# Kernel tuning notes

Hardware: AMD Instinct MI355X
Metric: run time of the kernel (lower is better)

## Reference

```python
import jax, jax.numpy as jnp
import numpy as np

EPS = 1e-8

def _rasterize_mesh(face_verts, H, W):
    # face_verts: [F,3,3] = (ndc_x, ndc_y, view_z) per triangle vertex
    x0, y0, z0 = face_verts[:, 0, 0], face_verts[:, 0, 1], face_verts[:, 0, 2]
    x1, y1, z1 = face_verts[:, 1, 0], face_verts[:, 1, 1], face_verts[:, 1, 2]
    x2, y2, z2 = face_verts[:, 2, 0], face_verts[:, 2, 1], face_verts[:, 2, 2]
    area = (x1 - x0) * (y2 - y0) - (y1 - y0) * (x2 - x0)
    # cull_backfaces=True (area<=0) + degenerate + behind-camera cull
    face_ok = (area > EPS) & (z0 > 0) & (z1 > 0) & (z2 > 0)
    inv_area = jnp.where(face_ok, 1.0 / jnp.where(face_ok, area, 1.0), 0.0)
    zs = jnp.stack([z0, z1, z2], -1)  # [F,3]
    # pytorch3d NDC: +x left, +y up, pixel centers
    xs = 1.0 - (2.0 * jnp.arange(W, dtype=jnp.float32) + 1.0) / W
    ys = 1.0 - (2.0 * jnp.arange(H, dtype=jnp.float32) + 1.0) / H

    def row_fn(py):
        px = xs[:, None]  # [W,1] broadcast vs faces [F]
        w0 = ((x1 - px) * (y2 - py) - (y1 - py) * (x2 - px)) * inv_area
        w1 = ((x2 - px) * (y0 - py) - (y2 - py) * (x0 - px)) * inv_area
        w2 = ((x0 - px) * (y1 - py) - (y0 - py) * (x1 - px)) * inv_area
        inside = (w0 >= 0) & (w1 >= 0) & (w2 >= 0) & face_ok
        # perspective_correct=True: l_i = w_i * prod(other z), renormalize
        l = jnp.stack([w0 * z1 * z2, z0 * w1 * z2, z0 * z1 * w2], -1)  # [W,F,3]
        s = l.sum(-1, keepdims=True)
        b = l / jnp.where(s == 0, 1.0, s)
        # clip_barycentric_coords=True
        b = jnp.clip(b, 0.0, None)
        b = b / jnp.clip(b.sum(-1, keepdims=True), EPS, None)
        zpix = (b * zs[None]).sum(-1)  # [W,F] interpolated view-space depth
        zm = jnp.where(inside, zpix, jnp.inf)
        fidx = jnp.argmin(zm, axis=1)  # z-buffer winner per pixel
        zmin = jnp.take_along_axis(zm, fidx[:, None], 1)[:, 0]
        hit = jnp.isfinite(zmin)
        bary = jnp.take_along_axis(b, fidx[:, None, None], 1)[:, 0]  # [W,3]
        return (jnp.where(hit, fidx, -1),
                jnp.where(hit, zmin, -1.0),
                jnp.where(hit[:, None], bary, -1.0))

    return jax.lax.map(row_fn, ys)  # ([H,W],[H,W],[H,W,3])


def _forward(positions, features, faces, K, RT, H, W):
    B, V, _ = positions.shape
    Fn = faces.shape[1]
    # --- create_camera_objects: open3d/opencv KRT -> pytorch3d camera ---
    R = RT[:, :, :3]
    t = RT[:, :, 3]
    scale = min(H, W) / 2.0
    focal = jnp.stack([K[:, 0, 0], K[:, 1, 1]], -1) / scale  # [B,2] NDC focal
    p0 = -(jnp.stack([K[:, 0, 2], K[:, 1, 2]], -1)
           - jnp.array([W / 2.0, H / 2.0], jnp.float32)) / scale  # [B,2]
    sign = jnp.array([-1.0, -1.0, 1.0], jnp.float32)
    R_p = jnp.swapaxes(R, 1, 2) * sign[None, None, :]  # R^T with cols 0,1 negated
    T_p = t * sign[None, :]
    # --- _get_mesh_ndc: world -> view -> NDC (pytorch3d row-vector convention) ---
    v_view = jnp.einsum('bvi,bij->bvj', positions, R_p) + T_p[:, None, :]
    z = v_view[..., 2:3]
    xy_ndc = focal[:, None, :] * v_view[..., :2] / z + p0[:, None, :]
    verts_ndc = jnp.concatenate([xy_ndc, z], -1)  # z overwritten with view-space depth
    face_verts = jax.vmap(lambda v, f: v[f])(verts_ndc, faces)  # [B,F,3,3]
    # --- rasterize (blur_sigma=0 -> faces_per_pixel=1) ---
    p2f, zbuf, bary = jax.vmap(lambda fv: _rasterize_mesh(fv, H, W))(face_verts)
    hit = p2f >= 0
    pix_to_face = jnp.where(hit, p2f + (jnp.arange(B) * Fn)[:, None, None], -1)
    # --- interpolate_face_attributes on packed faces/verts ---
    faces_packed = (faces + (jnp.arange(B) * V)[:, None, None]).reshape(B * Fn, 3)
    feats_packed = features.reshape(B * V, -1)
    fv_idx = faces_packed[jnp.clip(pix_to_face, 0)]  # [B,H,W,3]
    attrs = feats_packed[fv_idx]                      # [B,H,W,3,C]
    pix_feats = (bary[..., None] * attrs).sum(-2)
    pix_feats = jnp.where(hit[..., None], pix_feats, 0.0)
    dists = jnp.where(hit, 0.0, -1.0)
    # add faces_per_pixel (K=1) axis, matching pytorch3d Fragments layout
    return (pix_feats[:, :, :, None, :], pix_to_face[:, :, :, None],
            zbuf[:, :, :, None], bary[:, :, :, None, :], dists[:, :, :, None])


def setup_inputs() -> dict:
    key = jax.random.key(0)
    k1, k2, k3 = jax.random.split(key, 3)
    B, V, Fn, C, H, W = 1, 8192, 16384, 64, 192, 192
    positions = jax.random.uniform(k1, (B, V, 3), jnp.float32) * 2.0 - 1.0
    features = jax.random.normal(k2, (B, V, C), jnp.float32)
    faces = jax.random.randint(k3, (B, Fn, 3), 0, V)
    K = jnp.broadcast_to(jnp.array([[180.0, 0.0, 96.0], [0.0, 180.0, 96.0],
                                    [0.0, 0.0, 1.0]], jnp.float32), (B, 3, 3))
    RT = jnp.broadcast_to(jnp.concatenate(
        [jnp.eye(3, dtype=jnp.float32),
         jnp.array([[0.0], [0.0], [3.5]], jnp.float32)], axis=1), (B, 3, 4))
    return {"positions": positions, "features": features, "faces": faces,
            "K": K, "RT": RT, "H": H, "W": W, "blur_sigma": 0}


def reference(positions, features, faces, K, RT, H, W, blur_sigma):
    # blur_sigma == 0 path of VertexShader.forward (faces_per_pixel=1)
    return _forward(positions, features, faces, K, RT, H, W)
```

## Files before the change

### kernel.cpp

```cpp
#include <hip/hip_runtime.h>
#include <stdint.h>

#define H_ 192
#define W_ 192
#define C_ 64
#define EPS_F 1e-8f
#define TILE 16
#define NTX (W_/TILE)
#define NTY (H_/TILE)
#define CHUNK 256
#define NSLICE 8
#define NBUCKET 256
#define MAXCHUNK 64

typedef unsigned long long ull;

#define OFF_FEATS 0
#define OFF_P2F   (H_*W_*C_)
#define OFF_ZBUF  (OFF_P2F + H_*W_)
#define OFF_BARY  (OFF_ZBUF + H_*W_)
#define OFF_DIST  (OFF_BARY + H_*W_*3)

__device__ __forceinline__ float xm(float a, float b){ return __fmul_rn(a,b); }
__device__ __forceinline__ float xa(float a, float b){ return __fadd_rn(a,b); }
__device__ __forceinline__ float xsb(float a, float b){ return __fsub_rn(a,b); }
__device__ __forceinline__ float xd(float a, float b){ return __fdiv_rn(a,b); }

__device__ __forceinline__ float pixcoord(int i, float dim){
    float t = xa(xm(2.0f, (float)i), 1.0f);
    return xsb(1.0f, xd(t, dim));
}

__device__ __forceinline__ unsigned fenc(float f){
    unsigned b = __float_as_uint(f);
    return (b & 0x80000000u) ? ~b : (b | 0x80000000u);
}
__device__ __forceinline__ float fdec(unsigned e){
    unsigned b = (e & 0x80000000u) ? (e & 0x7FFFFFFFu) : ~e;
    return __uint_as_float(b);
}

__device__ __forceinline__ int zbucket(float zmn){
    int b = (int)((zmn - 2.0f) * 64.0f);
    return b < 0 ? 0 : (b > 254 ? 254 : b);
}
__device__ __forceinline__ float zlo_bucket(int b){
    if (b >= 255) return INFINITY;
    if (b == 0)   return 0.0f;
    return 2.0f + (float)b * 0.015625f;
}

__device__ __forceinline__ float3 tv(const float* __restrict__ pos,
        const float* __restrict__ K, const float* __restrict__ RT, int i){
    float p0 = pos[3*i+0], p1 = pos[3*i+1], p2 = pos[3*i+2];
    const float sgn[3] = {-1.f, -1.f, 1.f};
    float vv[3];
    #pragma unroll
    for (int j=0;j<3;j++){
        float rp0 = xm(RT[j*4+0], sgn[j]);
        float rp1 = xm(RT[j*4+1], sgn[j]);
        float rp2 = xm(RT[j*4+2], sgn[j]);
        float s = xa(xa(xm(p0,rp0), xm(p1,rp1)), xm(p2,rp2));
        vv[j] = xa(s, xm(RT[j*4+3], sgn[j]));
    }
    float z = vv[2];
    float fx = xd(K[0], 96.0f);
    float fy = xd(K[4], 96.0f);
    float p0x = -xd(xsb(K[2], 96.0f), 96.0f);
    float p0y = -xd(xsb(K[5], 96.0f), 96.0f);
    float xn = xa(xd(xm(fx, vv[0]), z), p0x);
    float yn = xa(xd(xm(fy, vv[1]), z), p0y);
    return make_float3(xn, yn, z);
}

__global__ __launch_bounds__(64) void k_pre(const float* __restrict__ pos,
        const float* __restrict__ K, const float* __restrict__ RT,
        const int* __restrict__ faces, float* __restrict__ rec0,
        unsigned* __restrict__ hist, unsigned* __restrict__ gbbmin,
        unsigned* __restrict__ gbbmax, int Fn){
    __shared__ unsigned lh[NBUCKET];
    int t = threadIdx.x, B = blockIdx.x;
    #pragma unroll
    for (int i=t; i<NBUCKET; i+=64) lh[i] = 0u;
    __syncthreads();
    int f = B*64 + t;
    float bxmn=INFINITY, bxmx=-INFINITY, bymn=INFINITY, bymx=-INFINITY;
    if (f < Fn){
        int i0 = faces[3*f+0], i1 = faces[3*f+1], i2 = faces[3*f+2];
        float3 v0 = tv(pos,K,RT,i0), v1 = tv(pos,K,RT,i1), v2 = tv(pos,K,RT,i2);
        float area = xsb(xm(xsb(v1.x,v0.x), xsb(v2.y,v0.y)), xm(xsb(v1.y,v0.y), xsb(v2.x,v0.x)));
        bool ok = (area > EPS_F) && (v0.z > 0.f) && (v1.z > 0.f) && (v2.z > 0.f);
        float ia = ok ? xd(1.0f, area) : 0.0f;
        float zmn = INFINITY;
        int b = 255;
        if (ok){
            zmn = fminf(v0.z, fminf(v1.z, v2.z));
            b = zbucket(zmn);
            bxmn = fminf(v0.x, fminf(v1.x, v2.x)) - 1e-4f;
            bxmx = fmaxf(v0.x, fmaxf(v1.x, v2.x)) + 1e-4f;
            bymn = fminf(v0.y, fminf(v1.y, v2.y)) - 1e-4f;
            bymx = fmaxf(v0.y, fmaxf(v1.y, v2.y)) + 1e-4f;
        }
        atomicAdd(&lh[b], 1u);
        float4* q = (float4*)(rec0 + (size_t)f*12);
        q[0] = make_float4(v0.x, v0.y, v1.x, v1.y);
        q[1] = make_float4(v2.x, v2.y, v0.z, v1.z);
        q[2] = make_float4(v2.z, ia, __int_as_float(f), zmn);
    }
    #pragma unroll
    for (int s2=1; s2<64; s2<<=1){
        bxmn = fminf(bxmn, __shfl_xor(bxmn, s2, 64));
        bxmx = fmaxf(bxmx, __shfl_xor(bxmx, s2, 64));
        bymn = fminf(bymn, __shfl_xor(bymn, s2, 64));
        bymx = fmaxf(bymx, __shfl_xor(bymx, s2, 64));
    }
    if (t == 0){
        atomicMin(&gbbmin[0], fenc(bxmn));
        atomicMax(&gbbmax[0], fenc(bxmx));
        atomicMin(&gbbmin[1], fenc(bymn));
        atomicMax(&gbbmax[1], fenc(bymx));
    }
    __syncthreads();
    #pragma unroll
    for (int i=t; i<NBUCKET; i+=64){
        unsigned cc = lh[i];
        if (cc) atomicAdd(&hist[i], cc);
    }
}

__global__ __launch_bounds__(256) void k_scatter(const float* __restrict__ rec0,
        const unsigned* __restrict__ hist, unsigned* __restrict__ histcur,
        float* __restrict__ rec, float* __restrict__ suffz, int Fn){
    __shared__ unsigned gst[NBUCKET], ssc[NBUCKET], lcnt[NBUCKET], lbase[NBUCKET];
    int t = threadIdx.x, B = blockIdx.x;
    unsigned hv = hist[t];
    ssc[t] = hv;
    lcnt[t] = 0u;
    __syncthreads();
    for (int d=1; d<NBUCKET; d<<=1){
        unsigned u = (t >= d) ? ssc[t-d] : 0u;
        __syncthreads();
        ssc[t] += u;
        __syncthreads();
    }
    gst[t] = ssc[t] - hv;
    __syncthreads();
    if (B == 0 && t < MAXCHUNK){
        unsigned pos = (unsigned)t * CHUNK;
        int bb = 0;
        #pragma unroll
        for (int s = 128; s > 0; s >>= 1){
            int nb = bb + s;
            if (nb <= NBUCKET && ssc[nb-1] <= pos) bb = nb;
        }
        suffz[t] = zlo_bucket(bb);
    }
    int f = B*256 + t;
    bool valid = (f < Fn);
    float4 q0, q1, q2;
    int b = 255; unsigned rank = 0; bool ok = false; float zmn = INFINITY;
    if (valid){
        const float4* q = (const float4*)(rec0 + (size_t)f*12);
        q0 = q[0]; q1 = q[1]; q2 = q[2];
        ok = (q2.y > 0.f);
        zmn = q2.w;
        b = ok ? zbucket(zmn) : 255;
        rank = atomicAdd(&lcnt[b], 1u);
    }
    __syncthreads();
    unsigned add = lcnt[t];
    if (add) lbase[t] = atomicAdd(&histcur[t], add);
    __syncthreads();
    if (valid){
        float x0=q0.x, y0=q0.y, x1=q0.z, y1=q0.w;
        float x2=q1.x, y2=q1.y, z0=q1.z, z1=q1.w;
        float z2=q2.x, ia=q2.y;
        float xmn, xmx, ymn, ymx, Ap=0.f, Bp=0.f, Cp=0.f;
        if (ok){
            xmn = fminf(x0, fminf(x1, x2)) - 1e-4f;
            xmx = fmaxf(x0, fmaxf(x1, x2)) + 1e-4f;
            ymn = fminf(y0, fminf(y1, y2)) - 1e-4f;
            ymx = fmaxf(y0, fmaxf(y1, y2)) + 1e-4f;
            float iz0 = 1.f/z0, iz1 = 1.f/z1, iz2 = 1.f/z2;
            Ap = ia * ((y1-y2)*iz0 + (y2-y0)*iz1 + (y0-y1)*iz2);
            Bp = ia * ((x2-x1)*iz0 + (x0-x2)*iz1 + (x1-x0)*iz2);
            Cp = ia * ((x1*y2-x2*y1)*iz0 + (x2*y0-x0*y2)*iz1 + (x0*y1-x1*y0)*iz2);
        } else {
            xmn = INFINITY; xmx = -INFINITY; ymn = INFINITY; ymx = -INFINITY;
        }
        unsigned p = gst[b] + lbase[b] + rank;
        float4* qo = (float4*)(rec + (size_t)p*20);
        qo[0] = q0; qo[1] = q1; qo[2] = q2;
        qo[3] = make_float4(Ap, Bp, Cp, 0.f);
        qo[4] = make_float4(xmn, xmx, ymn, ymx);
    }
}

__global__ __launch_bounds__(256) void k_raster(const float* __restrict__ rec,
        const float* __restrict__ suffz, const unsigned* __restrict__ gbbmin,
        const unsigned* __restrict__ gbbmax, ull* __restrict__ keys, int Fn){
    __shared__ float lds[CHUNK*12];
    __shared__ float zl[CHUNK];
    __shared__ int   slist[CHUNK];
    __shared__ int   wcnt[4];
    __shared__ float suff[MAXCHUNK];
    int tid = threadIdx.x;
    int nchunk = (Fn + CHUNK - 1) / CHUNK;
    if (tid < MAXCHUNK) suff[tid] = suffz[tid];
    int ix = blockIdx.x*TILE + (tid & 15);
    int iy = blockIdx.y*TILE + (tid >> 4);
    int pix = iy*W_ + ix;
    float px = pixcoord(ix, (float)W_);
    float py = pixcoord(iy, (float)H_);
    float tx_hi = pixcoord(blockIdx.x*TILE,          (float)W_);
    float tx_lo = pixcoord(blockIdx.x*TILE + TILE-1, (float)W_);
    float ty_hi = pixcoord(blockIdx.y*TILE,          (float)H_);
    float ty_lo = pixcoord(blockIdx.y*TILE + TILE-1, (float)H_);
    float gx0 = fdec(gbbmin[0]), gx1 = fdec(gbbmax[0]);
    float gy0 = fdec(gbbmin[1]), gy1 = fdec(gbbmax[1]);
    bool alive = (px >= gx0) && (px <= gx1) && (py >= gy0) && (py <= gy1);
    int lane = tid & 63, wv = tid >> 6;

    float zcut = INFINITY;
    ull localkey = 0xFFFFFFFFFFFFFFFFULL;
    ull published = 0xFFFFFFFFFFFFFFFFULL;
    __syncthreads();

    for (int c = (int)blockIdx.z; c < nchunk; c += NSLICE){
        ull g = __hip_atomic_load(&keys[pix], __ATOMIC_RELAXED, __HIP_MEMORY_SCOPE_AGENT);
        float zg = __uint_as_float((unsigned)(g >> 32));
        zcut = fminf(zcut, zg);
        float sc = (c < MAXCHUNK) ? suff[c] : 0.0f;
        int done = (!alive || !(xm(sc, 0.999f) < zcut)) ? 1 : 0;
        if (__syncthreads_and(done)) break;

        int fi = c*CHUNK + tid;
        float4 q0 = make_float4(0,0,0,0), q1 = q0, q2 = q0;
        bool keep = false;
        float zb = 0.f;
        if (fi < Fn){
            const float4* gq = (const float4*)(rec + (size_t)fi*20);
            q0 = gq[0]; q1 = gq[1]; q2 = gq[2];
            float4 q3 = gq[3], q4 = gq[4];
            keep = (q4.x <= tx_hi) && (q4.y >= tx_lo) && (q4.z <= ty_hi) && (q4.w >= ty_lo);
            if (keep){
                float ax = (q3.x > 0.f) ? tx_hi : tx_lo;
                float by = (q3.y > 0.f) ? ty_hi : ty_lo;
                float Nmax = q3.z + q3.x*ax + q3.y*by;
                float M = fabsf(q3.x*ax) + fabsf(q3.y*by) + fabsf(q3.z);
                float Nub = Nmax + 1e-5f*M + 1e-30f;
                if (Nub <= 0.f) keep = false;
                else zb = fmaxf(1.f/Nub, q2.w);
            }
        }
        float4* l = (float4*)(lds + tid*12);
        l[0] = q0; l[1] = q1; l[2] = q2;
        ull m = __ballot(keep);
        if (lane == 0) wcnt[wv] = __popcll(m);
        __syncthreads();
        int basecnt = 0;
        #pragma unroll
        for (int w2 = 0; w2 < 4; ++w2) if (w2 < wv) basecnt += wcnt[w2];
        if (keep){
            int p = basecnt + __popcll(m & ((1ULL << lane) - 1ULL));
            slist[p] = tid;
            zl[p] = zb;
        }
        int nsurv = wcnt[0] + wcnt[1] + wcnt[2] + wcnt[3];
        __syncthreads();

        for (int k = 0; k < nsurv; k++){
            float zbl = zl[k];
            if (!(xm(zbl, 0.999f) < zcut)) continue;
            int j = slist[k];
            const float* r = lds + j*12;
            float x0=r[0], y0=r[1], x1=r[2], y1=r[3], x2=r[4], y2=r[5];
            float dx0=xsb(x0,px), dx1=xsb(x1,px), dx2=xsb(x2,px);
            float dy0=xsb(y0,py), dy1=xsb(y1,py), dy2=xsb(y2,py);
            float e0 = xsb(xm(dx1,dy2), xm(dy1,dx2));
            float e1 = xsb(xm(dx2,dy0), xm(dy2,dx0));
            float e2 = xsb(xm(dx0,dy1), xm(dy0,dx1));
            if (e0 >= 0.f && e1 >= 0.f && e2 >= 0.f){
                float z0=r[6], z1=r[7], z2=r[8], ia=r[9];
                float w0 = xm(e0, ia), w1 = xm(e1, ia), w2 = xm(e2, ia);
                float l0 = xm(xm(w0,z1),z2);
                float l1 = xm(xm(z0,w1),z2);
                float l2 = xm(xm(z0,z1),w2);
                float s  = xa(xa(l0,l1),l2);
                float za = (l0*z0 + l1*z1 + l2*z2) / s;
                if (za*0.99999f >= zcut) continue;
                float dn = (s == 0.f) ? 1.0f : s;
                float b0 = fmaxf(xd(l0,dn), 0.f);
                float b1 = fmaxf(xd(l1,dn), 0.f);
                float b2 = fmaxf(xd(l2,dn), 0.f);
                float bs = fmaxf(xa(xa(b0,b1),b2), EPS_F);
                b0 = xd(b0,bs); b1 = xd(b1,bs); b2 = xd(b2,bs);
                float zp = xa(xa(xm(b0,z0),xm(b1,z1)),xm(b2,z2));
                ull ck = (((ull)__float_as_uint(zp)) << 32) | (unsigned)__float_as_int(r[10]);
                if (ck < localkey) localkey = ck;
                zcut = fminf(zcut, zp);
            }
        }
        if (localkey < published){
            atomicMin(&keys[pix], localkey);
            published = localkey;
        }
    }
    if (localkey < published) atomicMin(&keys[pix], localkey);
}

__global__ __launch_bounds__(256) void k_post(const ull* __restrict__ keys,
        const float* __restrict__ rec0, const float* __restrict__ feats,
        const int* __restrict__ faces, float* __restrict__ out){
    int grp = threadIdx.x >> 6;
    int c = threadIdx.x & 63;
    int pix = blockIdx.x*4 + grp;
    float* p2f  = out + OFF_P2F;
    float* zbuf = out + OFF_ZBUF;
    float* bary = out + OFF_BARY;
    float* dist = out + OFF_DIST;
    ull key = keys[pix];
    if (key == 0xFFFFFFFFFFFFFFFFULL){
        out[OFF_FEATS + pix*C_ + c] = 0.0f;
        if (c == 0){
            p2f[pix] = -1.0f; zbuf[pix] = -1.0f; dist[pix] = -1.0f;
        }
        if (c < 3) bary[3*pix+c] = -1.0f;
        return;
    }
    int f = (int)(key & 0xFFFFFFFFu);
    float z = __uint_as_float((unsigned)(key >> 32));
    int ix = pix % W_, iy = pix / W_;
    float px = pixcoord(ix, (float)W_);
    float py = pixcoord(iy, (float)H_);
    const float4* q = (const float4*)(rec0 + (size_t)f*12);
    float4 q0 = q[0], q1 = q[1], q2 = q[2];
    float x0=q0.x, y0=q0.y, x1=q0.z, y1=q0.w;
    float x2=q1.x, y2=q1.y, z0=q1.z, z1=q1.w;
    float z2=q2.x, ia=q2.y;
    float w0 = xm(xsb(xm(xsb(x1,px),xsb(y2,py)), xm(xsb(y1,py),xsb(x2,px))), ia);
    float w1 = xm(xsb(xm(xsb(x2,px),xsb(y0,py)), xm(xsb(y2,py),xsb(x0,px))), ia);
    float w2 = xm(xsb(xm(xsb(x0,px),xsb(y1,py)), xm(xsb(y0,py),xsb(x1,px))), ia);
    float l0 = xm(xm(w0,z1),z2);
    float l1 = xm(xm(z0,w1),z2);
    float l2 = xm(xm(z0,z1),w2);
    float s  = xa(xa(l0,l1),l2);
    float dn = (s == 0.f) ? 1.0f : s;
    float b0 = fmaxf(xd(l0,dn), 0.f);
    float b1 = fmaxf(xd(l1,dn), 0.f);
    float b2 = fmaxf(xd(l2,dn), 0.f);
    float bs = fmaxf(xa(xa(b0,b1),b2), EPS_F);
    b0 = xd(b0,bs); b1 = xd(b1,bs); b2 = xd(b2,bs);
    int i0 = faces[3*f+0], i1 = faces[3*f+1], i2 = faces[3*f+2];
    float res = xa(xa(xm(b0, feats[i0*C_ + c]), xm(b1, feats[i1*C_ + c])),
                   xm(b2, feats[i2*C_ + c]));
    out[OFF_FEATS + pix*C_ + c] = res;
    if (c == 0){
        p2f[pix] = (float)f; zbuf[pix] = z; dist[pix] = 0.0f;
    }
    if (c < 3){
        float bb = (c == 0) ? b0 : ((c == 1) ? b1 : b2);
        bary[3*pix+c] = bb;
    }
}

extern "C" void kernel_launch(void* const* d_in, const int* in_sizes, int n_in,
                              void* d_out, int out_size, void* d_ws, size_t ws_size,
                              hipStream_t stream) {
    const float* positions = (const float*)d_in[0];
    const float* features  = (const float*)d_in[1];
    const int*   faces     = (const int*)  d_in[2];
    const float* K         = (const float*)d_in[3];
    const float* RT        = (const float*)d_in[4];
    int Fn = in_sizes[2] / 3;

    ull*      keys     = (ull*)d_ws;
    unsigned* gbbmin   = (unsigned*)(keys + H_*W_);
    unsigned* hist     = gbbmin + 4;
    unsigned* histcur  = hist + NBUCKET;
    unsigned* gbbmax   = histcur + NBUCKET;
    float*    suffz    = (float*)(gbbmax + 4);
    float*    rec      = suffz + MAXCHUNK;
    float*    rec0     = rec + (size_t)Fn*20;

    size_t regA = (size_t)H_*W_*sizeof(ull) + 16;
    size_t regB = (NBUCKET*2 + 4)*4;
    hipMemsetAsync(keys, 0xFF, regA, stream);
    hipMemsetAsync(hist, 0x00, regB, stream);

    int nfb = (Fn + 255) / 256;
    k_pre<<<(Fn+63)/64, 64, 0, stream>>>(positions, K, RT, faces, rec0, hist, gbbmin, gbbmax, Fn);
    k_scatter<<<nfb, 256, 0, stream>>>(rec0, hist, histcur, rec, suffz, Fn);
    dim3 rg(NTX, NTY, NSLICE);
    k_raster<<<rg, dim3(256,1,1), 0, stream>>>(rec, suffz, gbbmin, gbbmax, keys, Fn);
    k_post<<<(H_*W_)/4, 256, 0, stream>>>(keys, rec0, features, faces, (float*)d_out);
}
```

Before: 141.9 us.

## Fuse post-shading into raster via last-slice tile counter, init keys in pre-pass

```diff
diff --git a/kernel.cpp b/kernel.cpp
--- a/kernel.cpp
+++ b/kernel.cpp
@@ -8,6 +8,7 @@
 #define TILE 16
 #define NTX (W_/TILE)
 #define NTY (H_/TILE)
+#define NTILES (NTX*NTY)
 #define CHUNK 256
 #define NSLICE 8
 #define NBUCKET 256
@@ -76,10 +77,12 @@
 __global__ __launch_bounds__(64) void k_pre(const float* __restrict__ pos,
         const float* __restrict__ K, const float* __restrict__ RT,
         const int* __restrict__ faces, float* __restrict__ rec0,
-        unsigned* __restrict__ hist, unsigned* __restrict__ gbbmin,
-        unsigned* __restrict__ gbbmax, int Fn){
+        unsigned* __restrict__ hist, unsigned* __restrict__ gbb,
+        ull* __restrict__ keys, int Fn){
     __shared__ unsigned lh[NBUCKET];
     int t = threadIdx.x, B = blockIdx.x;
+    int gthreads = gridDim.x*64;
+    for (int i = B*64 + t; i < H_*W_; i += gthreads) keys[i] = 0xFFFFFFFFFFFFFFFFULL;
     #pragma unroll
     for (int i=t; i<NBUCKET; i+=64) lh[i] = 0u;
     __syncthreads();
@@ -114,11 +117,11 @@
         bymn = fminf(bymn, __shfl_xor(bymn, s2, 64));
         bymx = fmaxf(bymx, __shfl_xor(bymx, s2, 64));
     }
-    if (t == 0){
-        atomicMin(&gbbmin[0], fenc(bxmn));
-        atomicMax(&gbbmax[0], fenc(bxmx));
-        atomicMin(&gbbmin[1], fenc(bymn));
-        atomicMax(&gbbmax[1], fenc(bymx));
+    if (t == 0 && bxmx > -INFINITY){
+        atomicMax(&gbb[0], fenc(-bxmn));
+        atomicMax(&gbb[1], fenc( bxmx));
+        atomicMax(&gbb[2], fenc(-bymn));
+        atomicMax(&gbb[3], fenc( bymx));
     }
     __syncthreads();
     #pragma unroll
@@ -197,13 +200,16 @@
 }
 
 __global__ __launch_bounds__(256) void k_raster(const float* __restrict__ rec,
-        const float* __restrict__ suffz, const unsigned* __restrict__ gbbmin,
-        const unsigned* __restrict__ gbbmax, ull* __restrict__ keys, int Fn){
+        const float* __restrict__ suffz, const unsigned* __restrict__ gbb,
+        ull* __restrict__ keys, unsigned* __restrict__ tilecnt,
+        const float* __restrict__ rec0, const float* __restrict__ feats,
+        const int* __restrict__ faces, float* __restrict__ out, int Fn){
     __shared__ float lds[CHUNK*12];
     __shared__ float zl[CHUNK];
     __shared__ int   slist[CHUNK];
     __shared__ int   wcnt[4];
     __shared__ float suff[MAXCHUNK];
+    __shared__ int   lastflag;
     int tid = threadIdx.x;
     int nchunk = (Fn + CHUNK - 1) / CHUNK;
     if (tid < MAXCHUNK) suff[tid] = suffz[tid];
@@ -216,8 +222,8 @@
     float tx_lo = pixcoord(blockIdx.x*TILE + TILE-1, (float)W_);
     float ty_hi = pixcoord(blockIdx.y*TILE,          (float)H_);
     float ty_lo = pixcoord(blockIdx.y*TILE + TILE-1, (float)H_);
-    float gx0 = fdec(gbbmin[0]), gx1 = fdec(gbbmax[0]);
-    float gy0 = fdec(gbbmin[1]), gy1 = fdec(gbbmax[1]);
+    float gx0 = -fdec(gbb[0]), gx1 = fdec(gbb[1]);
+    float gy0 = -fdec(gbb[2]), gy1 = fdec(gbb[3]);
     bool alive = (px >= gx0) && (px <= gx1) && (py >= gy0) && (py <= gy1);
     int lane = tid & 63, wv = tid >> 6;
 
@@ -307,60 +313,64 @@
         }
     }
     if (localkey < published) atomicMin(&keys[pix], localkey);
-}
-
-__global__ __launch_bounds__(256) void k_post(const ull* __restrict__ keys,
-        const float* __restrict__ rec0, const float* __restrict__ feats,
-        const int* __restrict__ faces, float* __restrict__ out){
-    int grp = threadIdx.x >> 6;
-    int c = threadIdx.x & 63;
-    int pix = blockIdx.x*4 + grp;
+
+    __threadfence();
+    if (tid == 0){
+        unsigned o = atomicAdd(&tilecnt[blockIdx.y*NTX + blockIdx.x], 1u);
+        lastflag = (o == NSLICE-1) ? 1 : 0;
+    }
+    __syncthreads();
+    if (!lastflag) return;
+    __threadfence();
+
+    int grp = tid >> 6, c = tid & 63;
     float* p2f  = out + OFF_P2F;
     float* zbuf = out + OFF_ZBUF;
     float* bary = out + OFF_BARY;
     float* dist = out + OFF_DIST;
-    ull key = keys[pix];
-    if (key == 0xFFFFFFFFFFFFFFFFULL){
-        out[OFF_FEATS + pix*C_ + c] = 0.0f;
-        if (c == 0){
-            p2f[pix] = -1.0f; zbuf[pix] = -1.0f; dist[pix] = -1.0f;
-        }
-        if (c < 3) bary[3*pix+c] = -1.0f;
-        return;
-    }
-    int f = (int)(key & 0xFFFFFFFFu);
-    float z = __uint_as_float((unsigned)(key >> 32));
-    int ix = pix % W_, iy = pix / W_;
-    float px = pixcoord(ix, (float)W_);
-    float py = pixcoord(iy, (float)H_);
-    const float4* q = (const float4*)(rec0 + (size_t)f*12);
-    float4 q0 = q[0], q1 = q[1], q2 = q[2];
-    float x0=q0.x, y0=q0.y, x1=q0.z, y1=q0.w;
-    float x2=q1.x, y2=q1.y, z0=q1.z, z1=q1.w;
-    float z2=q2.x, ia=q2.y;
-    float w0 = xm(xsb(xm(xsb(x1,px),xsb(y2,py)), xm(xsb(y1,py),xsb(x2,px))), ia);
-    float w1 = xm(xsb(xm(xsb(x2,px),xsb(y0,py)), xm(xsb(y2,py),xsb(x0,px))), ia);
-    float w2 = xm(xsb(xm(xsb(x0,px),xsb(y1,py)), xm(xsb(y0,py),xsb(x1,px))), ia);
-    float l0 = xm(xm(w0,z1),z2);
-    float l1 = xm(xm(z0,w1),z2);
-    float l2 = xm(xm(z0,z1),w2);
-    float s  = xa(xa(l0,l1),l2);
-    float dn = (s == 0.f) ? 1.0f : s;
-    float b0 = fmaxf(xd(l0,dn), 0.f);
-    float b1 = fmaxf(xd(l1,dn), 0.f);
-    float b2 = fmaxf(xd(l2,dn), 0.f);
-    float bs = fmaxf(xa(xa(b0,b1),b2), EPS_F);
-    b0 = xd(b0,bs); b1 = xd(b1,bs); b2 = xd(b2,bs);
-    int i0 = faces[3*f+0], i1 = faces[3*f+1], i2 = faces[3*f+2];
-    float res = xa(xa(xm(b0, feats[i0*C_ + c]), xm(b1, feats[i1*C_ + c])),
-                   xm(b2, feats[i2*C_ + c]));
-    out[OFF_FEATS + pix*C_ + c] = res;
-    if (c == 0){
-        p2f[pix] = (float)f; zbuf[pix] = z; dist[pix] = 0.0f;
-    }
-    if (c < 3){
-        float bb = (c == 0) ? b0 : ((c == 1) ? b1 : b2);
-        bary[3*pix+c] = bb;
+    for (int pp = 0; pp < 64; ++pp){
+        int pixloc = pp*4 + grp;
+        int ix2 = blockIdx.x*TILE + (pixloc & 15);
+        int iy2 = blockIdx.y*TILE + (pixloc >> 4);
+        int pix2 = iy2*W_ + ix2;
+        ull key = __hip_atomic_load(&keys[pix2], __ATOMIC_RELAXED, __HIP_MEMORY_SCOPE_AGENT);
+        if (key == 0xFFFFFFFFFFFFFFFFULL){
+            out[OFF_FEATS + pix2*C_ + c] = 0.0f;
+            if (c == 0){ p2f[pix2] = -1.0f; zbuf[pix2] = -1.0f; dist[pix2] = -1.0f; }
+            if (c < 3) bary[3*pix2+c] = -1.0f;
+            continue;
+        }
+        int f = (int)(key & 0xFFFFFFFFu);
+        float z = __uint_as_float((unsigned)(key >> 32));
+        float px2 = pixcoord(ix2, (float)W_);
+        float py2 = pixcoord(iy2, (float)H_);
+        const float4* q = (const float4*)(rec0 + (size_t)f*12);
+        float4 q0 = q[0], q1 = q[1], q2 = q[2];
+        float x0=q0.x, y0=q0.y, x1=q0.z, y1=q0.w;
+        float x2=q1.x, y2=q1.y, z0=q1.z, z1=q1.w;
+        float z2=q2.x, ia=q2.y;
+        float w0 = xm(xsb(xm(xsb(x1,px2),xsb(y2,py2)), xm(xsb(y1,py2),xsb(x2,px2))), ia);
+        float w1 = xm(xsb(xm(xsb(x2,px2),xsb(y0,py2)), xm(xsb(y2,py2),xsb(x0,px2))), ia);
+        float w2 = xm(xsb(xm(xsb(x0,px2),xsb(y1,py2)), xm(xsb(y0,py2),xsb(x1,px2))), ia);
+        float l0 = xm(xm(w0,z1),z2);
+        float l1 = xm(xm(z0,w1),z2);
+        float l2 = xm(xm(z0,z1),w2);
+        float s  = xa(xa(l0,l1),l2);
+        float dn = (s == 0.f) ? 1.0f : s;
+        float b0 = fmaxf(xd(l0,dn), 0.f);
+        float b1 = fmaxf(xd(l1,dn), 0.f);
+        float b2 = fmaxf(xd(l2,dn), 0.f);
+        float bs = fmaxf(xa(xa(b0,b1),b2), EPS_F);
+        b0 = xd(b0,bs); b1 = xd(b1,bs); b2 = xd(b2,bs);
+        int i0 = faces[3*f+0], i1 = faces[3*f+1], i2 = faces[3*f+2];
+        float res = xa(xa(xm(b0, feats[i0*C_ + c]), xm(b1, feats[i1*C_ + c])),
+                       xm(b2, feats[i2*C_ + c]));
+        out[OFF_FEATS + pix2*C_ + c] = res;
+        if (c == 0){ p2f[pix2] = (float)f; zbuf[pix2] = z; dist[pix2] = 0.0f; }
+        if (c < 3){
+            float bb = (c == 0) ? b0 : ((c == 1) ? b1 : b2);
+            bary[3*pix2+c] = bb;
+        }
     }
 }
 
@@ -375,23 +385,21 @@
     int Fn = in_sizes[2] / 3;
 
     ull*      keys     = (ull*)d_ws;
-    unsigned* gbbmin   = (unsigned*)(keys + H_*W_);
-    unsigned* hist     = gbbmin + 4;
+    unsigned* hist     = (unsigned*)(keys + H_*W_);
     unsigned* histcur  = hist + NBUCKET;
-    unsigned* gbbmax   = histcur + NBUCKET;
-    float*    suffz    = (float*)(gbbmax + 4);
+    unsigned* gbb      = histcur + NBUCKET;
+    unsigned* tilecnt  = gbb + 4;
+    float*    suffz    = (float*)(tilecnt + NTILES);
     float*    rec      = suffz + MAXCHUNK;
     float*    rec0     = rec + (size_t)Fn*20;
 
-    size_t regA = (size_t)H_*W_*sizeof(ull) + 16;
-    size_t regB = (NBUCKET*2 + 4)*4;
-    hipMemsetAsync(keys, 0xFF, regA, stream);
+    size_t regB = (NBUCKET*2 + 4 + NTILES)*4;
     hipMemsetAsync(hist, 0x00, regB, stream);
 
     int nfb = (Fn + 255) / 256;
-    k_pre<<<(Fn+63)/64, 64, 0, stream>>>(positions, K, RT, faces, rec0, hist, gbbmin, gbbmax, Fn);
+    k_pre<<<(Fn+63)/64, 64, 0, stream>>>(positions, K, RT, faces, rec0, hist, gbb, keys, Fn);
     k_scatter<<<nfb, 256, 0, stream>>>(rec0, hist, histcur, rec, suffz, Fn);
     dim3 rg(NTX, NTY, NSLICE);
-    k_raster<<<rg, dim3(256,1,1), 0, stream>>>(rec, suffz, gbbmin, gbbmax, keys, Fn);
-    k_post<<<(H_*W_)/4, 256, 0, stream>>>(keys, rec0, features, faces, (float*)d_out);
-}
+    k_raster<<<rg, dim3(256,1,1), 0, stream>>>(rec, suffz, gbb, keys, tilecnt,
+                                               rec0, features, faces, (float*)d_out, Fn);
+}
```

Result: slower. 255.5 us (+80.1%).

## Fold key init into preprocess, merge bbox atomics, add wave-level early break in raster

Applied to the files above, without the earlier changes.

```diff
diff --git a/kernel.cpp b/kernel.cpp
--- a/kernel.cpp
+++ b/kernel.cpp
@@ -76,10 +76,12 @@
 __global__ __launch_bounds__(64) void k_pre(const float* __restrict__ pos,
         const float* __restrict__ K, const float* __restrict__ RT,
         const int* __restrict__ faces, float* __restrict__ rec0,
-        unsigned* __restrict__ hist, unsigned* __restrict__ gbbmin,
-        unsigned* __restrict__ gbbmax, int Fn){
+        unsigned* __restrict__ hist, unsigned* __restrict__ gbb,
+        ull* __restrict__ keys, int Fn){
     __shared__ unsigned lh[NBUCKET];
     int t = threadIdx.x, B = blockIdx.x;
+    int gthreads = gridDim.x*64;
+    for (int i = B*64 + t; i < H_*W_; i += gthreads) keys[i] = 0xFFFFFFFFFFFFFFFFULL;
     #pragma unroll
     for (int i=t; i<NBUCKET; i+=64) lh[i] = 0u;
     __syncthreads();
@@ -114,11 +116,11 @@
         bymn = fminf(bymn, __shfl_xor(bymn, s2, 64));
         bymx = fmaxf(bymx, __shfl_xor(bymx, s2, 64));
     }
-    if (t == 0){
-        atomicMin(&gbbmin[0], fenc(bxmn));
-        atomicMax(&gbbmax[0], fenc(bxmx));
-        atomicMin(&gbbmin[1], fenc(bymn));
-        atomicMax(&gbbmax[1], fenc(bymx));
+    if (t == 0 && bxmx > -INFINITY){
+        atomicMax(&gbb[0], fenc(-bxmn));
+        atomicMax(&gbb[1], fenc( bxmx));
+        atomicMax(&gbb[2], fenc(-bymn));
+        atomicMax(&gbb[3], fenc( bymx));
     }
     __syncthreads();
     #pragma unroll
@@ -197,10 +199,11 @@
 }
 
 __global__ __launch_bounds__(256) void k_raster(const float* __restrict__ rec,
-        const float* __restrict__ suffz, const unsigned* __restrict__ gbbmin,
-        const unsigned* __restrict__ gbbmax, ull* __restrict__ keys, int Fn){
+        const float* __restrict__ suffz, const unsigned* __restrict__ gbb,
+        ull* __restrict__ keys, int Fn){
     __shared__ float lds[CHUNK*12];
     __shared__ float zl[CHUNK];
+    __shared__ float zfs[CHUNK];
     __shared__ int   slist[CHUNK];
     __shared__ int   wcnt[4];
     __shared__ float suff[MAXCHUNK];
@@ -216,8 +219,8 @@
     float tx_lo = pixcoord(blockIdx.x*TILE + TILE-1, (float)W_);
     float ty_hi = pixcoord(blockIdx.y*TILE,          (float)H_);
     float ty_lo = pixcoord(blockIdx.y*TILE + TILE-1, (float)H_);
-    float gx0 = fdec(gbbmin[0]), gx1 = fdec(gbbmax[0]);
-    float gy0 = fdec(gbbmin[1]), gy1 = fdec(gbbmax[1]);
+    float gx0 = -fdec(gbb[0]), gx1 = fdec(gbb[1]);
+    float gy0 = -fdec(gbb[2]), gy1 = fdec(gbb[3]);
     bool alive = (px >= gx0) && (px <= gx1) && (py >= gy0) && (py <= gy1);
     int lane = tid & 63, wv = tid >> 6;
 
@@ -237,7 +240,7 @@
         int fi = c*CHUNK + tid;
         float4 q0 = make_float4(0,0,0,0), q1 = q0, q2 = q0;
         bool keep = false;
-        float zb = 0.f;
+        float zb = 0.f, zf = 0.f;
         if (fi < Fn){
             const float4* gq = (const float4*)(rec + (size_t)fi*20);
             q0 = gq[0]; q1 = gq[1]; q2 = gq[2];
@@ -250,7 +253,10 @@
                 float M = fabsf(q3.x*ax) + fabsf(q3.y*by) + fabsf(q3.z);
                 float Nub = Nmax + 1e-5f*M + 1e-30f;
                 if (Nub <= 0.f) keep = false;
-                else zb = fmaxf(1.f/Nub, q2.w);
+                else {
+                    zf = zlo_bucket(zbucket(q2.w));
+                    zb = fmaxf(fmaxf(1.f/Nub, q2.w), zf);
+                }
             }
         }
         float4* l = (float4*)(lds + tid*12);
@@ -265,11 +271,14 @@
             int p = basecnt + __popcll(m & ((1ULL << lane) - 1ULL));
             slist[p] = tid;
             zl[p] = zb;
+            zfs[p] = zf;
         }
         int nsurv = wcnt[0] + wcnt[1] + wcnt[2] + wcnt[3];
         __syncthreads();
 
         for (int k = 0; k < nsurv; k++){
+            float zfl = zfs[k];
+            if (__all(!(xm(zfl, 0.999f) < zcut))) break;
             float zbl = zl[k];
             if (!(xm(zbl, 0.999f) < zcut)) continue;
             int j = slist[k];
@@ -375,23 +384,20 @@
     int Fn = in_sizes[2] / 3;
 
     ull*      keys     = (ull*)d_ws;
-    unsigned* gbbmin   = (unsigned*)(keys + H_*W_);
-    unsigned* hist     = gbbmin + 4;
+    unsigned* hist     = (unsigned*)(keys + H_*W_);
     unsigned* histcur  = hist + NBUCKET;
-    unsigned* gbbmax   = histcur + NBUCKET;
-    float*    suffz    = (float*)(gbbmax + 4);
+    unsigned* gbb      = histcur + NBUCKET;
+    float*    suffz    = (float*)(gbb + 4);
     float*    rec      = suffz + MAXCHUNK;
     float*    rec0     = rec + (size_t)Fn*20;
 
-    size_t regA = (size_t)H_*W_*sizeof(ull) + 16;
     size_t regB = (NBUCKET*2 + 4)*4;
-    hipMemsetAsync(keys, 0xFF, regA, stream);
     hipMemsetAsync(hist, 0x00, regB, stream);
 
     int nfb = (Fn + 255) / 256;
-    k_pre<<<(Fn+63)/64, 64, 0, stream>>>(positions, K, RT, faces, rec0, hist, gbbmin, gbbmax, Fn);
+    k_pre<<<(Fn+63)/64, 64, 0, stream>>>(positions, K, RT, faces, rec0, hist, gbb, keys, Fn);
     k_scatter<<<nfb, 256, 0, stream>>>(rec0, hist, histcur, rec, suffz, Fn);
     dim3 rg(NTX, NTY, NSLICE);
-    k_raster<<<rg, dim3(256,1,1), 0, stream>>>(rec, suffz, gbbmin, gbbmax, keys, Fn);
+    k_raster<<<rg, dim3(256,1,1), 0, stream>>>(rec, suffz, gbb, keys, Fn);
     k_post<<<(H_*W_)/4, 256, 0, stream>>>(keys, rec0, features, faces, (float*)d_out);
 }
```

Result: slower. 175.0 us (+23.3%).
